# Optimization experiments

Hardware: AMD Instinct MI355X
Metric: run time of the kernel (lower is better)

## Reference

```python
import jax, jax.numpy as jnp
import numpy as np

N_NODES = 100000


def gcn_conv(x, W, b, src, dst, num_nodes):
    """PyG GCNConv: out = D^{-1/2} (A + I) D^{-1/2} (x W) + b, messages src->dst."""
    h = x @ W  # [N, out]
    # degree with self-loops (edge weight 1)
    deg = jax.ops.segment_sum(jnp.ones(src.shape[0], dtype=x.dtype), dst,
                              num_segments=num_nodes) + 1.0
    dinv = jax.lax.rsqrt(deg)  # [N]
    norm = dinv[src] * dinv[dst]  # [E]
    msg = h[src] * norm[:, None]  # gather + scale, [E, out]
    agg = jax.ops.segment_sum(msg, dst, num_segments=num_nodes)
    # self-loop term: norm_ii = dinv[i]^2
    agg = agg + h * (dinv * dinv)[:, None]
    return agg + b


def setup_inputs() -> dict:
    key = jax.random.key(0)
    ks = jax.random.split(key, 9)
    N, F_in, H1, H2, C = N_NODES, 128, 64, 32, 10
    E = 3200000
    feature = jax.random.normal(ks[0], (N, F_in), dtype=jnp.float32)
    edge_index = jax.random.randint(ks[1], (2, E), 0, N, dtype=jnp.int64)
    def glorot(k, shape):
        lim = np.sqrt(6.0 / (shape[0] + shape[1]))
        return jax.random.uniform(k, shape, jnp.float32, -lim, lim)
    return {
        "feature": feature,
        "edge_index": edge_index,
        "W1": glorot(ks[2], (F_in, H1)),
        "b1": jnp.zeros((H1,), jnp.float32),
        "W2": glorot(ks[3], (H1, H2)),
        "b2": jnp.zeros((H2,), jnp.float32),
        "Wc": glorot(ks[4], (H2, C)),
        "bc": jnp.zeros((C,), jnp.float32),
    }


def reference(feature, edge_index, W1, b1, W2, b2, Wc, bc):
    src, dst = edge_index[0], edge_index[1]
    x = gcn_conv(feature, W1, b1, src, dst, N_NODES)
    x = jax.nn.relu(x)
    # dropout is identity in eval mode
    x = gcn_conv(x, W2, b2, src, dst, N_NODES)
    x = jax.nn.relu(x)
    logits = x @ Wc + bc
    return jax.nn.log_softmax(logits, axis=1)
```

## Files before the change

### kernel.cpp

```cpp
#include <hip/hip_runtime.h>

#define N_NODES 100000
#define F_IN 128
#define H1 64
#define H2 32
#define NCLS 10

#define BS_N 256
#define NBUCK ((N_NODES + BS_N - 1) / BS_N)
#define LCAP 32
#define MCAP 9216
#define OVCAP 6144
#define STCAP 9216
#define BIN_WG 256

typedef _Float16 h2_t __attribute__((ext_vector_type(2)));
typedef _Float16 f16x8 __attribute__((ext_vector_type(8)));
typedef float f32x4 __attribute__((ext_vector_type(4)));

__device__ __forceinline__ float fdot2u(unsigned int u, h2_t sel, float c) {
    return __builtin_amdgcn_fdot2(__builtin_bit_cast(h2_t, u), sel, c, false);
}
__device__ __forceinline__ void accd4(float* a, uint4 v, h2_t lo, h2_t hi) {
    a[0] = fdot2u(v.x, lo, a[0]); a[1] = fdot2u(v.x, hi, a[1]);
    a[2] = fdot2u(v.y, lo, a[2]); a[3] = fdot2u(v.y, hi, a[3]);
    a[4] = fdot2u(v.z, lo, a[4]); a[5] = fdot2u(v.z, hi, a[5]);
    a[6] = fdot2u(v.w, lo, a[6]); a[7] = fdot2u(v.w, hi, a[7]);
}
__device__ __forceinline__ unsigned int pkh(float a, float b) {
    return __builtin_bit_cast(unsigned int, __builtin_amdgcn_cvt_pkrtz(a, b));
}

__global__ __launch_bounds__(512) void bin_kernel(const int* __restrict__ src,
                                                  const int* __restrict__ dst, int E,
                                                  unsigned int* __restrict__ gcur,
                                                  unsigned int* __restrict__ mainr,
                                                  unsigned int* __restrict__ ovcnt,
                                                  unsigned int* __restrict__ ovbuf) {
    __shared__ unsigned int buf[NBUCK][LCAP + 1];
    __shared__ int cnt[NBUCK];
    int tid = threadIdx.x;
    for (int b = tid; b < NBUCK; b += 512) cnt[b] = 0;

    int chunk = (E + gridDim.x - 1) / gridDim.x;
    int e_lo = blockIdx.x * chunk;
    int e_hi = min(e_lo + chunk, E);

    int d[4], s[4];
    #pragma unroll
    for (int k = 0; k < 4; ++k) {
        int e = e_lo + k * 512 + tid;
        d[k] = 0; s[k] = 0;
        if (e < e_hi) { d[k] = dst[e]; s[k] = src[e]; }
    }
    __syncthreads();

    for (int base = e_lo; base < e_hi; base += 2048) {
        #pragma unroll
        for (int k = 0; k < 4; ++k) {
            if (base + k * 512 + tid < e_hi) {
                int b = d[k] >> 8;
                unsigned int en = ((unsigned int)s[k] << 8) | (unsigned int)(d[k] & 255);
                int p = atomicAdd(&cnt[b], 1);
                if (p < LCAP) buf[b][p] = en;
                else {
                    unsigned int op = atomicAdd(&ovcnt[b * 16], 1u);
                    if (op < OVCAP) ovbuf[(size_t)b * OVCAP + op] = en;
                }
            }
        }
        __syncthreads();
        {
            int nb = base + 2048;
            #pragma unroll
            for (int k = 0; k < 4; ++k) {
                int e = nb + k * 512 + tid;
                if (e < e_hi) { d[k] = dst[e]; s[k] = src[e]; }
            }
        }
        for (int b = tid; b < NBUCK; b += 512) {
            int c = cnt[b]; if (c > LCAP) c = LCAP;
            int nf = c & ~15;
            if (nf) {
                unsigned int gb = atomicAdd(&gcur[b * 16], (unsigned int)nf);
                if (gb + (unsigned)nf <= MCAP) {
                    for (int k = 0; k < nf; k += 4) {
                        uint4 v = make_uint4(buf[b][k], buf[b][k + 1],
                                             buf[b][k + 2], buf[b][k + 3]);
                        *(uint4*)&mainr[(size_t)b * MCAP + gb + k] = v;
                    }
                } else {
                    unsigned int op = atomicAdd(&ovcnt[b * 16], (unsigned int)nf);
                    for (int k = 0; k < nf; ++k)
                        if (op + k < OVCAP) ovbuf[(size_t)b * OVCAP + op + k] = buf[b][k];
                }
                int rem = c - nf;
                for (int k = 0; k < rem; ++k) buf[b][k] = buf[b][nf + k];
                cnt[b] = rem;
            } else {
                cnt[b] = c;
            }
        }
        __syncthreads();
    }
    for (int b = tid; b < NBUCK; b += 512) {
        int c = cnt[b]; if (c > LCAP) c = LCAP;
        int nf = c & ~3;
        if (nf) {
            unsigned int gb = atomicAdd(&gcur[b * 16], (unsigned int)nf);
            if (gb + (unsigned)nf <= MCAP) {
                for (int k = 0; k < nf; k += 4) {
                    uint4 v = make_uint4(buf[b][k], buf[b][k + 1],
                                         buf[b][k + 2], buf[b][k + 3]);
                    *(uint4*)&mainr[(size_t)b * MCAP + gb + k] = v;
                }
            } else {
                unsigned int op = atomicAdd(&ovcnt[b * 16], (unsigned int)nf);
                for (int k = 0; k < nf; ++k)
                    if (op + k < OVCAP) ovbuf[(size_t)b * OVCAP + op + k] = buf[b][k];
            }
        }
        int rem = c - nf;
        if (rem) {
            unsigned int ob = atomicAdd(&ovcnt[b * 16], (unsigned int)rem);
            for (int k = 0; k < rem; ++k)
                if (ob + k < OVCAP) ovbuf[(size_t)b * OVCAP + ob + k] = buf[b][nf + k];
        }
    }
}

__global__ __launch_bounds__(512) void build_kernel(const unsigned int* __restrict__ gcur,
                                                    unsigned int* __restrict__ mainr,
                                                    const unsigned int* __restrict__ ovcnt,
                                                    const unsigned int* __restrict__ ovbuf,
                                                    float* __restrict__ dinv,
                                                    int2* __restrict__ row_se) {
    __shared__ unsigned int stage[STCAP];
    __shared__ unsigned int outb[STCAP];
    __shared__ int degl[BS_N];
    __shared__ int rs_l[BS_N];
    __shared__ int curl[BS_N];
    __shared__ int wtot[4];
    int b = blockIdx.x;
    int tid = threadIdx.x;

    int cm = (int)gcur[b * 16]; if (cm > MCAP) cm = MCAP;
    for (int i = tid; i < cm; i += 512) stage[i] = mainr[(size_t)b * MCAP + i];
    int co = (int)ovcnt[b * 16]; if (co > OVCAP) co = OVCAP;
    for (int i = tid; i < co; i += 512) {
        int p = cm + i;
        if (p < STCAP) stage[p] = ovbuf[(size_t)b * OVCAP + i];
    }
    int c = cm + co; if (c > STCAP) c = STCAP;
    if (tid < BS_N) degl[tid] = 0;
    __syncthreads();

    for (int i = tid; i < c; i += 512) atomicAdd(&degl[stage[i] & 255], 1);
    __syncthreads();

    if (tid < BS_N) {
        int lane = tid & 63, w = tid >> 6;
        int d = degl[tid];
        int x = d;
        #pragma unroll
        for (int off = 1; off < 64; off <<= 1) {
            int y = __shfl_up(x, off);
            if (lane >= off) x += y;
        }
        if (lane == 63) wtot[w] = x;
        __syncthreads();
        int pbase = 0;
        #pragma unroll
        for (int k = 0; k < 4; ++k) if (k < w) pbase += wtot[k];
        rs_l[tid] = pbase + x - d;
        curl[tid] = 0;
    } else {
        __syncthreads();
    }
    __syncthreads();

    for (int i = tid; i < c; i += 512) {
        unsigned int en = stage[i];
        int dl = en & 255;
        int p = atomicAdd(&curl[dl], 1);
        outb[rs_l[dl] + p] = en >> 8;
    }
    __syncthreads();
    size_t gbase = (size_t)b * MCAP;
    int c4 = (c + 3) >> 2;
    for (int i = tid; i < c4; i += 512)
        *(uint4*)&mainr[gbase + (size_t)i * 4] = *(const uint4*)&outb[i * 4];

    int node = b * BS_N + tid;
    if (tid < BS_N && node < N_NODES) {
        int deg = degl[tid];
        dinv[node] = rsqrtf((float)deg + 1.0f);
        int rs = (int)gbase + rs_l[tid];
        row_se[node] = make_int2(rs, rs + deg);
    }
}

__global__ __launch_bounds__(256) void gemm1_kernel(const float* __restrict__ X,
                                                    const float* __restrict__ W,
                                                    const float* __restrict__ dinv,
                                                    unsigned short* __restrict__ H) {
    __shared__ union {
        struct {
            _Float16 As[64][136];
            _Float16 Wf[16][64][8];
        } s;
        _Float16 Hs[64][72];
    } u;
    int r0 = blockIdx.x * 64;
    int tid = threadIdx.x;
    for (int i = tid; i < 2048; i += 256) {
        int row = i >> 5, k4 = i & 31;
        int grow = r0 + row;
        float4 v = (grow < N_NODES) ? ((const float4*)X)[(size_t)grow * 32 + k4]
                                    : make_float4(0.f, 0.f, 0.f, 0.f);
        _Float16 t4[4] = {(_Float16)v.x, (_Float16)v.y, (_Float16)v.z, (_Float16)v.w};
        *(uint2*)&u.s.As[row][k4 * 4] = *(uint2*)t4;
    }
    for (int i = tid; i < F_IN * H1; i += 256) {
        int k = i >> 6, col = i & 63;
        u.s.Wf[k >> 3][col][k & 7] = (_Float16)W[i];
    }
    __syncthreads();

    int lane = tid & 63, w = tid >> 6;
    int lr = lane & 15, lkg = lane >> 4;
    f32x4 acc[4] = {{0.f, 0.f, 0.f, 0.f}, {0.f, 0.f, 0.f, 0.f},
                    {0.f, 0.f, 0.f, 0.f}, {0.f, 0.f, 0.f, 0.f}};
    #pragma unroll
    for (int ks = 0; ks < 4; ++ks) {
        f16x8 a = *(const f16x8*)&u.s.As[w * 16 + lr][ks * 32 + lkg * 8];
        #pragma unroll
        for (int nt = 0; nt < 4; ++nt) {
            f16x8 bfr = *(const f16x8*)&u.s.Wf[ks * 4 + lkg][nt * 16 + lr][0];
            acc[nt] = __builtin_amdgcn_mfma_f32_16x16x32_f16(a, bfr, acc[nt], 0, 0, 0);
        }
    }
    __syncthreads();
    float dv[4];
    #pragma unroll
    for (int q = 0; q < 4; ++q) {
        int grow = r0 + w * 16 + lkg * 4 + q;
        dv[q] = (grow < N_NODES) ? dinv[grow] : 0.f;
    }
    #pragma unroll
    for (int nt = 0; nt < 4; ++nt)
        #pragma unroll
        for (int q = 0; q < 4; ++q)
            u.Hs[w * 16 + lkg * 4 + q][nt * 16 + lr] = (_Float16)(acc[nt][q] * dv[q]);
    __syncthreads();
    for (int i = tid; i < 512; i += 256) {
        int row = i >> 3, seg = i & 7;
        int grow = r0 + row;
        if (grow < N_NODES)
            *(uint4*)&H[(size_t)grow * H1 + seg * 8] = *(const uint4*)&u.Hs[row][seg * 8];
    }
}

__global__ __launch_bounds__(256) void gemm2_kernel(const float* __restrict__ X,
                                                    const float* __restrict__ W,
                                                    const float* __restrict__ dinv,
                                                    unsigned short* __restrict__ H) {
    __shared__ float Xs[64][68];
    __shared__ float Ws[H1 * H2];
    int r0 = blockIdx.x * 64;
    const float4* W4 = (const float4*)W;
    float4* Ws4 = (float4*)Ws;
    for (int i = threadIdx.x; i < H1 * H2 / 4; i += 256) Ws4[i] = W4[i];
    for (int it = 0; it < 4; ++it) {
        int idx = threadIdx.x + it * 256;
        int r = idx >> 4, k4 = idx & 15;
        int row = r0 + r;
        float4 v = (row < N_NODES)
            ? ((const float4*)X)[(size_t)row * 16 + k4]
            : make_float4(0.f, 0.f, 0.f, 0.f);
        *(float4*)&Xs[r][k4 * 4] = v;
    }
    __syncthreads();
    int tx = threadIdx.x & 15;
    int ty = threadIdx.x >> 4;
    float acc[4][2] = {};
    #pragma unroll 8
    for (int k = 0; k < 64; ++k) {
        float2 wb = *(const float2*)&Ws[k * H2 + tx * 2];
        float xa0 = Xs[ty * 4 + 0][k];
        float xa1 = Xs[ty * 4 + 1][k];
        float xa2 = Xs[ty * 4 + 2][k];
        float xa3 = Xs[ty * 4 + 3][k];
        acc[0][0] += xa0 * wb.x; acc[0][1] += xa0 * wb.y;
        acc[1][0] += xa1 * wb.x; acc[1][1] += xa1 * wb.y;
        acc[2][0] += xa2 * wb.x; acc[2][1] += xa2 * wb.y;
        acc[3][0] += xa3 * wb.x; acc[3][1] += xa3 * wb.y;
    }
    #pragma unroll
    for (int i = 0; i < 4; ++i) {
        int row = r0 + ty * 4 + i;
        if (row < N_NODES) {
            float dv = dinv[row];
            *(unsigned int*)&H[(size_t)row * H2 + tx * 2] = pkh(acc[i][0] * dv, acc[i][1] * dv);
        }
    }
}

__global__ __launch_bounds__(256) void pull1_kernel(const unsigned short* __restrict__ h,
                                                    const unsigned int* __restrict__ csr,
                                                    const int2* __restrict__ row_se,
                                                    const float* __restrict__ dinv,
                                                    const float* __restrict__ b,
                                                    float* __restrict__ xout) {
    int wave = (blockIdx.x * 256 + threadIdx.x) >> 6;
    int lane = threadIdx.x & 63;
    int g = lane >> 3;
    int sub = lane & 7;
    int i = wave;
    int2 se = row_se[i];
    int e0 = se.x, e1 = se.y;
    int deg = e1 - e0;
    const h2_t selo = {(_Float16)1.0f, (_Float16)0.0f};
    const h2_t sehi = {(_Float16)0.0f, (_Float16)1.0f};
    float acc[8] = {};
    if (deg <= 48) {
        int sidx = (int)csr[e0 + lane];
        int i0 = __shfl(sidx, g);
        int i1 = __shfl(sidx, 8 + g);
        int i2 = __shfl(sidx, 16 + g);
        int i3 = __shfl(sidx, 24 + g);
        int i4 = __shfl(sidx, 32 + g);
        int i5 = __shfl(sidx, 40 + g);
        bool p0 = (g < deg),      p1 = (8 + g < deg),  p2 = (16 + g < deg);
        bool p3 = (24 + g < deg), p4 = (32 + g < deg), p5 = (40 + g < deg);
        uint4 v0 = make_uint4(0u, 0u, 0u, 0u), v1 = v0, v2 = v0, v3 = v0, v4 = v0, v5 = v0;
        if (p0) v0 = *(const uint4*)&h[(size_t)i0 * H1 + sub * 8];
        if (p1) v1 = *(const uint4*)&h[(size_t)i1 * H1 + sub * 8];
        if (p2) v2 = *(const uint4*)&h[(size_t)i2 * H1 + sub * 8];
        if (p3) v3 = *(const uint4*)&h[(size_t)i3 * H1 + sub * 8];
        if (p4) v4 = *(const uint4*)&h[(size_t)i4 * H1 + sub * 8];
        if (p5) v5 = *(const uint4*)&h[(size_t)i5 * H1 + sub * 8];
        if (p0) accd4(acc, v0, selo, sehi);
        if (p1) accd4(acc, v1, selo, sehi);
        if (p2) accd4(acc, v2, selo, sehi);
        if (p3) accd4(acc, v3, selo, sehi);
        if (p4) accd4(acc, v4, selo, sehi);
        if (p5) accd4(acc, v5, selo, sehi);
    } else {
        int e = e0;
        for (; e + 16 <= e1; e += 16) {
            int s0 = csr[e + g];
            int s1 = csr[e + 8 + g];
            uint4 v0 = *(const uint4*)&h[(size_t)s0 * H1 + sub * 8];
            uint4 v1 = *(const uint4*)&h[(size_t)s1 * H1 + sub * 8];
            accd4(acc, v0, selo, sehi);
            accd4(acc, v1, selo, sehi);
        }
        if (e + 8 <= e1) {
            int s = csr[e + g];
            uint4 v = *(const uint4*)&h[(size_t)s * H1 + sub * 8];
            accd4(acc, v, selo, sehi);
            e += 8;
        }
        if (e < e1) {
            int idx = e + g;
            if (idx < e1) {
                int s = csr[idx];
                uint4 v = *(const uint4*)&h[(size_t)s * H1 + sub * 8];
                accd4(acc, v, selo, sehi);
            }
        }
    }
    #pragma unroll
    for (int m = 8; m < 64; m <<= 1) {
        #pragma unroll
        for (int j = 0; j < 8; ++j) acc[j] += __shfl_xor(acc[j], m);
    }
    if (g == 0) {
        float di = dinv[i];
        uint4 sv = *(const uint4*)&h[(size_t)i * H1 + sub * 8];
        accd4(acc, sv, selo, sehi);
        float4 bb0 = *(const float4*)&b[sub * 8];
        float4 bb1 = *(const float4*)&b[sub * 8 + 4];
        float4 o0, o1;
        o0.x = fmaxf(di * acc[0] + bb0.x, 0.0f);
        o0.y = fmaxf(di * acc[1] + bb0.y, 0.0f);
        o0.z = fmaxf(di * acc[2] + bb0.z, 0.0f);
        o0.w = fmaxf(di * acc[3] + bb0.w, 0.0f);
        o1.x = fmaxf(di * acc[4] + bb1.x, 0.0f);
        o1.y = fmaxf(di * acc[5] + bb1.y, 0.0f);
        o1.z = fmaxf(di * acc[6] + bb1.z, 0.0f);
        o1.w = fmaxf(di * acc[7] + bb1.w, 0.0f);
        *(float4*)&xout[(size_t)i * H1 + sub * 8] = o0;
        *(float4*)&xout[(size_t)i * H1 + sub * 8 + 4] = o1;
    }
}

__global__ __launch_bounds__(256) void pull2_kernel(const unsigned short* __restrict__ h,
                                                    const unsigned int* __restrict__ csr,
                                                    const int2* __restrict__ row_se,
                                                    const float* __restrict__ dinv,
                                                    const float* __restrict__ b,
                                                    float* __restrict__ xout) {
    int wave = (blockIdx.x * 256 + threadIdx.x) >> 6;
    int lane = threadIdx.x & 63;
    int g = lane >> 2;
    int sub = lane & 3;
    int i = wave;
    int2 se = row_se[i];
    int e0 = se.x, e1 = se.y;
    int deg = e1 - e0;
    const h2_t selo = {(_Float16)1.0f, (_Float16)0.0f};
    const h2_t sehi = {(_Float16)0.0f, (_Float16)1.0f};
    float acc[8] = {};
    if (deg <= 48) {
        int sidx = (int)csr[e0 + lane];
        int i0 = __shfl(sidx, g);
        int i1 = __shfl(sidx, 16 + g);
        int i2 = __shfl(sidx, 32 + g);
        bool p0 = (g < deg), p1 = (16 + g < deg), p2 = (32 + g < deg);
        uint4 v0 = make_uint4(0u, 0u, 0u, 0u), v1 = v0, v2 = v0;
        if (p0) v0 = *(const uint4*)&h[(size_t)i0 * H2 + sub * 8];
        if (p1) v1 = *(const uint4*)&h[(size_t)i1 * H2 + sub * 8];
        if (p2) v2 = *(const uint4*)&h[(size_t)i2 * H2 + sub * 8];
        if (p0) accd4(acc, v0, selo, sehi);
        if (p1) accd4(acc, v1, selo, sehi);
        if (p2) accd4(acc, v2, selo, sehi);
    } else {
        int e = e0;
        for (; e + 32 <= e1; e += 32) {
            int s0 = csr[e + g];
            int s1 = csr[e + 16 + g];
            uint4 v0 = *(const uint4*)&h[(size_t)s0 * H2 + sub * 8];
            uint4 v1 = *(const uint4*)&h[(size_t)s1 * H2 + sub * 8];
            accd4(acc, v0, selo, sehi);
            accd4(acc, v1, selo, sehi);
        }
        if (e + 16 <= e1) {
            int s = csr[e + g];
            uint4 v = *(const uint4*)&h[(size_t)s * H2 + sub * 8];
            accd4(acc, v, selo, sehi);
            e += 16;
        }
        if (e < e1) {
            int idx = e + g;
            if (idx < e1) {
                int s = csr[idx];
                uint4 v = *(const uint4*)&h[(size_t)s * H2 + sub * 8];
                accd4(acc, v, selo, sehi);
            }
        }
    }
    #pragma unroll
    for (int m = 4; m < 64; m <<= 1) {
        #pragma unroll
        for (int j = 0; j < 8; ++j) acc[j] += __shfl_xor(acc[j], m);
    }
    if (g == 0) {
        float di = dinv[i];
        uint4 sv = *(const uint4*)&h[(size_t)i * H2 + sub * 8];
        accd4(acc, sv, selo, sehi);
        float4 bb0 = *(const float4*)&b[sub * 8];
        float4 bb1 = *(const float4*)&b[sub * 8 + 4];
        float4 o0, o1;
        o0.x = fmaxf(di * acc[0] + bb0.x, 0.0f);
        o0.y = fmaxf(di * acc[1] + bb0.y, 0.0f);
        o0.z = fmaxf(di * acc[2] + bb0.z, 0.0f);
        o0.w = fmaxf(di * acc[3] + bb0.w, 0.0f);
        o1.x = fmaxf(di * acc[4] + bb1.x, 0.0f);
        o1.y = fmaxf(di * acc[5] + bb1.y, 0.0f);
        o1.z = fmaxf(di * acc[6] + bb1.z, 0.0f);
        o1.w = fmaxf(di * acc[7] + bb1.w, 0.0f);
        *(float4*)&xout[(size_t)i * H2 + sub * 8] = o0;
        *(float4*)&xout[(size_t)i * H2 + sub * 8 + 4] = o1;
    }
}

__global__ __launch_bounds__(256) void final_kernel(const float* __restrict__ X2,
                                                    const float* __restrict__ Wc,
                                                    const float* __restrict__ bc,
                                                    float* __restrict__ out) {
    __shared__ float Ws[H2 * NCLS];
    __shared__ float bs[NCLS];
    for (int idx = threadIdx.x; idx < H2 * NCLS; idx += 256) Ws[idx] = Wc[idx];
    if (threadIdx.x < NCLS) bs[threadIdx.x] = bc[threadIdx.x];
    __syncthreads();
    int i = blockIdx.x * blockDim.x + threadIdx.x;
    if (i >= N_NODES) return;
    float x[H2];
    #pragma unroll
    for (int k = 0; k < H2; ++k) x[k] = X2[(size_t)i * H2 + k];
    float lg[NCLS];
    #pragma unroll
    for (int c = 0; c < NCLS; ++c) {
        float acc = bs[c];
        #pragma unroll
        for (int k = 0; k < H2; ++k) acc += x[k] * Ws[k * NCLS + c];
        lg[c] = acc;
    }
    float m = lg[0];
    #pragma unroll
    for (int c = 1; c < NCLS; ++c) m = fmaxf(m, lg[c]);
    float s = 0.0f;
    #pragma unroll
    for (int c = 0; c < NCLS; ++c) s += expf(lg[c] - m);
    float lse = m + logf(s);
    #pragma unroll
    for (int c = 0; c < NCLS; ++c) out[(size_t)i * NCLS + c] = lg[c] - lse;
}

extern "C" void kernel_launch(void* const* d_in, const int* in_sizes, int n_in,
                              void* d_out, int out_size, void* d_ws, size_t ws_size,
                              hipStream_t stream) {
    const float* feature = (const float*)d_in[0];
    const int*   eidx    = (const int*)d_in[1];
    const float* W1      = (const float*)d_in[2];
    const float* b1      = (const float*)d_in[3];
    const float* W2      = (const float*)d_in[4];
    const float* b2      = (const float*)d_in[5];
    const float* Wc      = (const float*)d_in[6];
    const float* bc      = (const float*)d_in[7];
    float* out = (float*)d_out;

    const int E = in_sizes[1] / 2;
    const int* src = eidx;
    const int* dst = eidx + E;

    float*          ws        = (float*)d_ws;
    float*          dinv      = ws;
    int2*           row_se    = (int2*)(dinv + N_NODES);
    unsigned int*   gcur      = (unsigned int*)(row_se + N_NODES);
    unsigned int*   ovcnt     = gcur + (size_t)NBUCK * 16;
    unsigned int*   ovbuf     = ovcnt + (size_t)NBUCK * 16;
    unsigned int*   mainr     = ovbuf + (size_t)NBUCK * OVCAP;
    unsigned short* h1b       = (unsigned short*)(mainr + (size_t)NBUCK * MCAP);
    float*          x1        = (float*)(h1b + (size_t)N_NODES * H1);
    unsigned short* h2b       = h1b;
    float*          x2        = x1;

    hipMemsetAsync(gcur, 0, (size_t)NBUCK * 32 * sizeof(unsigned int), stream);
    bin_kernel<<<BIN_WG, 512, 0, stream>>>(src, dst, E, gcur, mainr, ovcnt, ovbuf);
    build_kernel<<<NBUCK, 512, 0, stream>>>(gcur, mainr, ovcnt, ovbuf, dinv, row_se);

    gemm1_kernel<<<(N_NODES + 63) / 64, 256, 0, stream>>>(feature, W1, dinv, h1b);
    {
        unsigned int grid = (unsigned int)(((size_t)N_NODES * 64 + 255) / 256);
        pull1_kernel<<<grid, 256, 0, stream>>>(h1b, mainr, row_se, dinv, b1, x1);
    }

    gemm2_kernel<<<(N_NODES + 63) / 64, 256, 0, stream>>>(x1, W2, dinv, h2b);
    {
        unsigned int grid = (unsigned int)(((size_t)N_NODES * 64 + 255) / 256);
        pull2_kernel<<<grid, 256, 0, stream>>>(h2b, mainr, row_se, dinv, b2, x2);
    }

    final_kernel<<<(N_NODES + 255) / 256, 256, 0, stream>>>(x2, Wc, bc, out);
}
```

Baseline: 272.8 us.

## Fuse CSR bucket build with first-layer GEMM into one kernel

Merges the per-bucket CSR build kernel with the layer-1 feature GEMM. Each build block now also computes x@W1 for its 256 nodes in two 128-row MFMA tiles, reusing the shared-memory region and taking dinv from LDS instead of global memory. This removes one kernel launch and the global round trip for dinv. In exchange the fused block is longer and uses more LDS, and gemm2_kernel is only moved in the file.

```diff
diff --git a/kernel.cpp b/kernel.cpp
--- a/kernel.cpp
+++ b/kernel.cpp
@@ -129,33 +129,42 @@
     }
 }
 
-__global__ __launch_bounds__(512) void build_kernel(const unsigned int* __restrict__ gcur,
-                                                    unsigned int* __restrict__ mainr,
-                                                    const unsigned int* __restrict__ ovcnt,
-                                                    const unsigned int* __restrict__ ovbuf,
-                                                    float* __restrict__ dinv,
-                                                    int2* __restrict__ row_se) {
-    __shared__ unsigned int stage[STCAP];
-    __shared__ unsigned int outb[STCAP];
+__global__ __launch_bounds__(512) void buildgemm1_kernel(const unsigned int* __restrict__ gcur,
+                                                         unsigned int* __restrict__ mainr,
+                                                         const unsigned int* __restrict__ ovcnt,
+                                                         const unsigned int* __restrict__ ovbuf,
+                                                         float* __restrict__ dinv,
+                                                         int2* __restrict__ row_se,
+                                                         const float* __restrict__ X,
+                                                         const float* __restrict__ W1,
+                                                         unsigned short* __restrict__ H) {
+    __shared__ union {
+        struct { unsigned int stage[STCAP]; unsigned int outb[STCAP]; } bu;
+        struct {
+            _Float16 Wf[16][64][8];
+            union { _Float16 As[128][136]; _Float16 Hs[128][72]; } t;
+        } g;
+    } u;
     __shared__ int degl[BS_N];
     __shared__ int rs_l[BS_N];
     __shared__ int curl[BS_N];
     __shared__ int wtot[4];
+    __shared__ float dinvl[BS_N];
     int b = blockIdx.x;
     int tid = threadIdx.x;
 
     int cm = (int)gcur[b * 16]; if (cm > MCAP) cm = MCAP;
-    for (int i = tid; i < cm; i += 512) stage[i] = mainr[(size_t)b * MCAP + i];
+    for (int i = tid; i < cm; i += 512) u.bu.stage[i] = mainr[(size_t)b * MCAP + i];
     int co = (int)ovcnt[b * 16]; if (co > OVCAP) co = OVCAP;
     for (int i = tid; i < co; i += 512) {
         int p = cm + i;
-        if (p < STCAP) stage[p] = ovbuf[(size_t)b * OVCAP + i];
+        if (p < STCAP) u.bu.stage[p] = ovbuf[(size_t)b * OVCAP + i];
     }
     int c = cm + co; if (c > STCAP) c = STCAP;
     if (tid < BS_N) degl[tid] = 0;
     __syncthreads();
 
-    for (int i = tid; i < c; i += 512) atomicAdd(&degl[stage[i] & 255], 1);
+    for (int i = tid; i < c; i += 512) atomicAdd(&degl[u.bu.stage[i] & 255], 1);
     __syncthreads();
 
     if (tid < BS_N) {
@@ -180,128 +189,75 @@
     __syncthreads();
 
     for (int i = tid; i < c; i += 512) {
-        unsigned int en = stage[i];
+        unsigned int en = u.bu.stage[i];
         int dl = en & 255;
         int p = atomicAdd(&curl[dl], 1);
-        outb[rs_l[dl] + p] = en >> 8;
+        u.bu.outb[rs_l[dl] + p] = en >> 8;
     }
     __syncthreads();
     size_t gbase = (size_t)b * MCAP;
     int c4 = (c + 3) >> 2;
     for (int i = tid; i < c4; i += 512)
-        *(uint4*)&mainr[gbase + (size_t)i * 4] = *(const uint4*)&outb[i * 4];
+        *(uint4*)&mainr[gbase + (size_t)i * 4] = *(const uint4*)&u.bu.outb[i * 4];
 
     int node = b * BS_N + tid;
-    if (tid < BS_N && node < N_NODES) {
+    if (tid < BS_N) {
         int deg = degl[tid];
-        dinv[node] = rsqrtf((float)deg + 1.0f);
-        int rs = (int)gbase + rs_l[tid];
-        row_se[node] = make_int2(rs, rs + deg);
-    }
-}
-
-__global__ __launch_bounds__(256) void gemm1_kernel(const float* __restrict__ X,
-                                                    const float* __restrict__ W,
-                                                    const float* __restrict__ dinv,
-                                                    unsigned short* __restrict__ H) {
-    __shared__ union {
-        struct {
-            _Float16 As[64][136];
-            _Float16 Wf[16][64][8];
-        } s;
-        _Float16 Hs[64][72];
-    } u;
-    int r0 = blockIdx.x * 64;
-    int tid = threadIdx.x;
-    for (int i = tid; i < 2048; i += 256) {
-        int row = i >> 5, k4 = i & 31;
-        int grow = r0 + row;
-        float4 v = (grow < N_NODES) ? ((const float4*)X)[(size_t)grow * 32 + k4]
-                                    : make_float4(0.f, 0.f, 0.f, 0.f);
-        _Float16 t4[4] = {(_Float16)v.x, (_Float16)v.y, (_Float16)v.z, (_Float16)v.w};
-        *(uint2*)&u.s.As[row][k4 * 4] = *(uint2*)t4;
-    }
-    for (int i = tid; i < F_IN * H1; i += 256) {
+        float dv = rsqrtf((float)deg + 1.0f);
+        dinvl[tid] = dv;
+        if (node < N_NODES) {
+            dinv[node] = dv;
+            int rs = (int)gbase + rs_l[tid];
+            row_se[node] = make_int2(rs, rs + deg);
+        }
+    }
+    __syncthreads();
+
+    for (int i = tid; i < F_IN * H1; i += 512) {
         int k = i >> 6, col = i & 63;
-        u.s.Wf[k >> 3][col][k & 7] = (_Float16)W[i];
-    }
-    __syncthreads();
-
+        u.g.Wf[k >> 3][col][k & 7] = (_Float16)W1[i];
+    }
     int lane = tid & 63, w = tid >> 6;
     int lr = lane & 15, lkg = lane >> 4;
-    f32x4 acc[4] = {{0.f, 0.f, 0.f, 0.f}, {0.f, 0.f, 0.f, 0.f},
-                    {0.f, 0.f, 0.f, 0.f}, {0.f, 0.f, 0.f, 0.f}};
-    #pragma unroll
-    for (int ks = 0; ks < 4; ++ks) {
-        f16x8 a = *(const f16x8*)&u.s.As[w * 16 + lr][ks * 32 + lkg * 8];
-        #pragma unroll
-        for (int nt = 0; nt < 4; ++nt) {
-            f16x8 bfr = *(const f16x8*)&u.s.Wf[ks * 4 + lkg][nt * 16 + lr][0];
-            acc[nt] = __builtin_amdgcn_mfma_f32_16x16x32_f16(a, bfr, acc[nt], 0, 0, 0);
-        }
-    }
-    __syncthreads();
-    float dv[4];
-    #pragma unroll
-    for (int q = 0; q < 4; ++q) {
-        int grow = r0 + w * 16 + lkg * 4 + q;
-        dv[q] = (grow < N_NODES) ? dinv[grow] : 0.f;
-    }
-    #pragma unroll
-    for (int nt = 0; nt < 4; ++nt)
-        #pragma unroll
-        for (int q = 0; q < 4; ++q)
-            u.Hs[w * 16 + lkg * 4 + q][nt * 16 + lr] = (_Float16)(acc[nt][q] * dv[q]);
-    __syncthreads();
-    for (int i = tid; i < 512; i += 256) {
-        int row = i >> 3, seg = i & 7;
-        int grow = r0 + row;
-        if (grow < N_NODES)
-            *(uint4*)&H[(size_t)grow * H1 + seg * 8] = *(const uint4*)&u.Hs[row][seg * 8];
-    }
-}
-
-__global__ __launch_bounds__(256) void gemm2_kernel(const float* __restrict__ X,
-                                                    const float* __restrict__ W,
-                                                    const float* __restrict__ dinv,
-                                                    unsigned short* __restrict__ H) {
-    __shared__ float Xs[64][68];
-    __shared__ float Ws[H1 * H2];
-    int r0 = blockIdx.x * 64;
-    const float4* W4 = (const float4*)W;
-    float4* Ws4 = (float4*)Ws;
-    for (int i = threadIdx.x; i < H1 * H2 / 4; i += 256) Ws4[i] = W4[i];
-    for (int it = 0; it < 4; ++it) {
-        int idx = threadIdx.x + it * 256;
-        int r = idx >> 4, k4 = idx & 15;
-        int row = r0 + r;
-        float4 v = (row < N_NODES)
-            ? ((const float4*)X)[(size_t)row * 16 + k4]
-            : make_float4(0.f, 0.f, 0.f, 0.f);
-        *(float4*)&Xs[r][k4 * 4] = v;
-    }
-    __syncthreads();
-    int tx = threadIdx.x & 15;
-    int ty = threadIdx.x >> 4;
-    float acc[4][2] = {};
-    #pragma unroll 8
-    for (int k = 0; k < 64; ++k) {
-        float2 wb = *(const float2*)&Ws[k * H2 + tx * 2];
-        float xa0 = Xs[ty * 4 + 0][k];
-        float xa1 = Xs[ty * 4 + 1][k];
-        float xa2 = Xs[ty * 4 + 2][k];
-        float xa3 = Xs[ty * 4 + 3][k];
-        acc[0][0] += xa0 * wb.x; acc[0][1] += xa0 * wb.y;
-        acc[1][0] += xa1 * wb.x; acc[1][1] += xa1 * wb.y;
-        acc[2][0] += xa2 * wb.x; acc[2][1] += xa2 * wb.y;
-        acc[3][0] += xa3 * wb.x; acc[3][1] += xa3 * wb.y;
-    }
-    #pragma unroll
-    for (int i = 0; i < 4; ++i) {
-        int row = r0 + ty * 4 + i;
-        if (row < N_NODES) {
-            float dv = dinv[row];
-            *(unsigned int*)&H[(size_t)row * H2 + tx * 2] = pkh(acc[i][0] * dv, acc[i][1] * dv);
+    #pragma unroll
+    for (int t = 0; t < 2; ++t) {
+        int r0 = b * BS_N + t * 128;
+        __syncthreads();
+        for (int i = tid; i < 4096; i += 512) {
+            int row = i >> 5, k4 = i & 31;
+            int grow = r0 + row;
+            float4 v = (grow < N_NODES) ? ((const float4*)X)[(size_t)grow * 32 + k4]
+                                        : make_float4(0.f, 0.f, 0.f, 0.f);
+            _Float16 t4[4] = {(_Float16)v.x, (_Float16)v.y, (_Float16)v.z, (_Float16)v.w};
+            *(uint2*)&u.g.t.As[row][k4 * 4] = *(uint2*)t4;
+        }
+        __syncthreads();
+        f32x4 acc[4] = {{0.f, 0.f, 0.f, 0.f}, {0.f, 0.f, 0.f, 0.f},
+                        {0.f, 0.f, 0.f, 0.f}, {0.f, 0.f, 0.f, 0.f}};
+        #pragma unroll
+        for (int ks = 0; ks < 4; ++ks) {
+            f16x8 a = *(const f16x8*)&u.g.t.As[w * 16 + lr][ks * 32 + lkg * 8];
+            #pragma unroll
+            for (int nt = 0; nt < 4; ++nt) {
+                f16x8 bfr = *(const f16x8*)&u.g.Wf[ks * 4 + lkg][nt * 16 + lr][0];
+                acc[nt] = __builtin_amdgcn_mfma_f32_16x16x32_f16(a, bfr, acc[nt], 0, 0, 0);
+            }
+        }
+        __syncthreads();
+        float dv[4];
+        #pragma unroll
+        for (int q = 0; q < 4; ++q) dv[q] = dinvl[t * 128 + w * 16 + lkg * 4 + q];
+        #pragma unroll
+        for (int nt = 0; nt < 4; ++nt)
+            #pragma unroll
+            for (int q = 0; q < 4; ++q)
+                u.g.t.Hs[w * 16 + lkg * 4 + q][nt * 16 + lr] = (_Float16)(acc[nt][q] * dv[q]);
+        __syncthreads();
+        for (int i = tid; i < 1024; i += 512) {
+            int row = i >> 3, seg = i & 7;
+            int grow = r0 + row;
+            if (grow < N_NODES)
+                *(uint4*)&H[(size_t)grow * H1 + seg * 8] = *(const uint4*)&u.g.t.Hs[row][seg * 8];
         }
     }
 }
@@ -396,6 +352,51 @@
     }
 }
 
+__global__ __launch_bounds__(256) void gemm2_kernel(const float* __restrict__ X,
+                                                    const float* __restrict__ W,
+                                                    const float* __restrict__ dinv,
+                                                    unsigned short* __restrict__ H) {
+    __shared__ float Xs[64][68];
+    __shared__ float Ws[H1 * H2];
+    int r0 = blockIdx.x * 64;
+    const float4* W4 = (const float4*)W;
+    float4* Ws4 = (float4*)Ws;
+    for (int i = threadIdx.x; i < H1 * H2 / 4; i += 256) Ws4[i] = W4[i];
+    for (int it = 0; it < 4; ++it) {
+        int idx = threadIdx.x + it * 256;
+        int r = idx >> 4, k4 = idx & 15;
+        int row = r0 + r;
+        float4 v = (row < N_NODES)
+            ? ((const float4*)X)[(size_t)row * 16 + k4]
+            : make_float4(0.f, 0.f, 0.f, 0.f);
+        *(float4*)&Xs[r][k4 * 4] = v;
+    }
+    __syncthreads();
+    int tx = threadIdx.x & 15;
+    int ty = threadIdx.x >> 4;
+    float acc[4][2] = {};
+    #pragma unroll 8
+    for (int k = 0; k < 64; ++k) {
+        float2 wb = *(const float2*)&Ws[k * H2 + tx * 2];
+        float xa0 = Xs[ty * 4 + 0][k];
+        float xa1 = Xs[ty * 4 + 1][k];
+        float xa2 = Xs[ty * 4 + 2][k];
+        float xa3 = Xs[ty * 4 + 3][k];
+        acc[0][0] += xa0 * wb.x; acc[0][1] += xa0 * wb.y;
+        acc[1][0] += xa1 * wb.x; acc[1][1] += xa1 * wb.y;
+        acc[2][0] += xa2 * wb.x; acc[2][1] += xa2 * wb.y;
+        acc[3][0] += xa3 * wb.x; acc[3][1] += xa3 * wb.y;
+    }
+    #pragma unroll
+    for (int i = 0; i < 4; ++i) {
+        int row = r0 + ty * 4 + i;
+        if (row < N_NODES) {
+            float dv = dinv[row];
+            *(unsigned int*)&H[(size_t)row * H2 + tx * 2] = pkh(acc[i][0] * dv, acc[i][1] * dv);
+        }
+    }
+}
+
 __global__ __launch_bounds__(256) void pull2_kernel(const unsigned short* __restrict__ h,
                                                     const unsigned int* __restrict__ csr,
                                                     const int2* __restrict__ row_se,
@@ -540,9 +541,9 @@
 
     hipMemsetAsync(gcur, 0, (size_t)NBUCK * 32 * sizeof(unsigned int), stream);
     bin_kernel<<<BIN_WG, 512, 0, stream>>>(src, dst, E, gcur, mainr, ovcnt, ovbuf);
-    build_kernel<<<NBUCK, 512, 0, stream>>>(gcur, mainr, ovcnt, ovbuf, dinv, row_se);
-
-    gemm1_kernel<<<(N_NODES + 63) / 64, 256, 0, stream>>>(feature, W1, dinv, h1b);
+    buildgemm1_kernel<<<NBUCK, 512, 0, stream>>>(gcur, mainr, ovcnt, ovbuf,
+                                                 dinv, row_se, feature, W1, h1b);
+
     {
         unsigned int grid = (unsigned int)(((size_t)N_NODES * 64 + 255) / 256);
         pull1_kernel<<<grid, 256, 0, stream>>>(h1b, mainr, row_se, dinv, b1, x1);
```

Result: no change. 276.6 us (+1.4%).
